# Optimization experiments

Measured on AMD Instinct MI355X. Metric: run time of the kernel, lower is better.

The kernel has to match this reference:

```python
import jax, jax.numpy as jnp
import numpy as np

B, DEC, ENC, HID, UNITS = 4, 256, 1024, 512, 128


def setup_inputs() -> dict:
    key = jax.random.key(0)
    k1, k2, k3, k4, k5, k6 = jax.random.split(key, 6)
    query = jax.random.normal(k1, (B, DEC, HID), dtype=jnp.float32)
    value = jax.random.normal(k2, (B, ENC, HID), dtype=jnp.float32)
    mask = jax.random.bernoulli(k3, 0.9, (B, ENC))  # bool, True = keep
    # Dense(units, use_bias=False) kernels, glorot-ish scaling
    W1 = jax.random.normal(k4, (HID, UNITS), dtype=jnp.float32) * (1.0 / np.sqrt(HID))
    W2 = jax.random.normal(k5, (HID, UNITS), dtype=jnp.float32) * (1.0 / np.sqrt(HID))
    # AdditiveAttention use_scale=True: learned per-unit scale vector
    scale = jax.random.normal(k6, (UNITS,), dtype=jnp.float32) * (1.0 / np.sqrt(UNITS))
    return {"query": query, "value": value, "mask": mask, "W1": W1, "W2": W2, "scale": scale}


def reference(query, value, mask, W1, W2, scale):
    # query: (B, DEC, HID), value: (B, ENC, HID), mask: (B, ENC) bool
    q = jnp.einsum("bqh,hu->bqu", query, W1)   # (B, DEC, U)
    k = jnp.einsum("beh,hu->beu", value, W2)   # (B, ENC, U)
    # Bahdanau additive score: sum_u scale_u * tanh(q + k)  -> (B, DEC, ENC)
    scores = jnp.einsum("bqeu,u->bqe", jnp.tanh(q[:, :, None, :] + k[:, None, :, :]), scale)
    neg = jnp.asarray(-1e9, scores.dtype)
    scores = jnp.where(mask[:, None, :], scores, neg)
    attention_weights = jax.nn.softmax(scores, axis=-1)   # (B, DEC, ENC)
    context_vector = jnp.einsum("bqe,beh->bqh", attention_weights, value)  # (B, DEC, HID)
    # query_mask is all-ones in the original module -> no-op on output
    return (context_vector, attention_weights)
```

## Files before the change

### kernel.cpp

```cpp
#include <hip/hip_runtime.h>
#include <cstddef>

#define B     4
#define DEC   256
#define ENC   1024
#define HID   512
#define UNITS 128

#define PROJ_SCALE 2.8853900817779268f

__global__ __launch_bounds__(256) void proj_kernel(
    const float* __restrict__ query, const float* __restrict__ value,
    const float* __restrict__ W1,    const float* __restrict__ W2,
    float* __restrict__ qbuf,        float* __restrict__ kbufT)
{
    __shared__ float part[4][8][UNITS];

    const int tid  = threadIdx.x;
    const int lane = tid & 63;
    const int wv   = __builtin_amdgcn_readfirstlane(tid >> 6);
    const int row0g = blockIdx.x * 8;
    const bool isQ = row0g < B * DEC;
    const float* X = isQ ? query : value;
    const float* W = isQ ? W1 : W2;
    const int row0 = isQ ? row0g : row0g - B * DEC;
    const int h0   = wv * 128;

    float acc0[8], acc1[8];
    #pragma unroll
    for (int r = 0; r < 8; ++r) { acc0[r] = 0.f; acc1[r] = 0.f; }

    const float* Xb = X + (size_t)row0 * HID + h0;
    const float* Wb = W + (size_t)h0 * UNITS;

    float wa[4], wb[4];
    #pragma unroll
    for (int j = 0; j < 4; ++j) {
        wa[j] = Wb[j * UNITS + lane];
        wb[j] = Wb[j * UNITS + 64 + lane];
    }

    for (int h = 0; h < 128; h += 4) {
        const int hp = (h + 4 < 128) ? h + 4 : h;
        float na[4], nb[4];
        #pragma unroll
        for (int j = 0; j < 4; ++j) {
            na[j] = Wb[(hp + j) * UNITS + lane];
            nb[j] = Wb[(hp + j) * UNITS + 64 + lane];
        }
        #pragma unroll
        for (int r = 0; r < 8; ++r) {
            const float4 xv = *(const float4*)(Xb + r * HID + h);
            acc0[r] += xv.x*wa[0] + xv.y*wa[1] + xv.z*wa[2] + xv.w*wa[3];
            acc1[r] += xv.x*wb[0] + xv.y*wb[1] + xv.z*wb[2] + xv.w*wb[3];
        }
        #pragma unroll
        for (int j = 0; j < 4; ++j) { wa[j] = na[j]; wb[j] = nb[j]; }
    }

    #pragma unroll
    for (int r = 0; r < 8; ++r) {
        part[wv][r][lane]      = acc0[r];
        part[wv][r][64 + lane] = acc1[r];
    }
    __syncthreads();

    #pragma unroll
    for (int k = 0; k < 4; ++k) {
        const int idx = tid + k * 256;
        const int r = idx >> 7, u = idx & (UNITS - 1);
        const float s = PROJ_SCALE *
            ((part[0][r][u] + part[1][r][u]) + (part[2][r][u] + part[3][r][u]));
        const int row = row0 + r;
        if (isQ) {
            qbuf[(size_t)row * UNITS + u] = s;
        } else {
            const int bb = row >> 10, e = row & (ENC - 1);
            const int c = u >> 2, j = u & 3;
            kbufT[((size_t)bb * 32 * ENC + (size_t)c * ENC + e) * 4 + j] = s;
        }
    }
}

__device__ __forceinline__ float sig_r(float a) {
    return __builtin_amdgcn_rcpf(1.f + __builtin_amdgcn_exp2f(a));
}

__global__ __launch_bounds__(1024) void score_kernel(
    const float* __restrict__ qbuf, const float* __restrict__ kbufT,
    const int* __restrict__ mask,   const float* __restrict__ scale,
    float* __restrict__ attn_out)
{
    const int bi  = blockIdx.x;
    const int b   = (bi >> 1) & 3;
    const int dq0 = (((bi >> 3) << 1) | (bi & 1)) * 2;
    const int tid = threadIdx.x;

    float S0 = 0.f;
    for (int j = 0; j < UNITS; j += 4) {
        const float4 sv = *(const float4*)(scale + j);
        S0 += (sv.x + sv.y) + (sv.z + sv.w);
    }

    const float* q0 = qbuf + (size_t)(b * DEC + dq0) * UNITS;
    const float* q1 = q0 + UNITS;
    const float* kc = kbufT + (size_t)b * 32 * ENC * 4 + (size_t)tid * 4;

    float t0 = 0.f, t1 = 0.f;

    float4 kv0 = *(const float4*)(kc + (size_t)0 * ENC * 4);
    float4 kv1 = *(const float4*)(kc + (size_t)1 * ENC * 4);
    float4 kv2 = *(const float4*)(kc + (size_t)2 * ENC * 4);
    float4 kv3 = *(const float4*)(kc + (size_t)3 * ENC * 4);

    for (int i = 0; i < 32; i += 4) {
        const int ip = (i + 4 < 32) ? (i + 4) : i;
        float4 n0 = *(const float4*)(kc + (size_t)(ip + 0) * ENC * 4);
        float4 n1 = *(const float4*)(kc + (size_t)(ip + 1) * ENC * 4);
        float4 n2 = *(const float4*)(kc + (size_t)(ip + 2) * ENC * 4);
        float4 n3 = *(const float4*)(kc + (size_t)(ip + 3) * ENC * 4);

        #pragma unroll
        for (int j = 0; j < 4; ++j) {
            const float4 kv = (j == 0) ? kv0 : (j == 1) ? kv1 : (j == 2) ? kv2 : kv3;
            const int ii = i + j;
            const float4 qa = *(const float4*)(q0 + ii * 4);
            const float4 qb = *(const float4*)(q1 + ii * 4);
            const float4 sv = *(const float4*)(scale + ii * 4);
            t0 += sv.x * sig_r(qa.x + kv.x);
            t0 += sv.y * sig_r(qa.y + kv.y);
            t0 += sv.z * sig_r(qa.z + kv.z);
            t0 += sv.w * sig_r(qa.w + kv.w);
            t1 += sv.x * sig_r(qb.x + kv.x);
            t1 += sv.y * sig_r(qb.y + kv.y);
            t1 += sv.z * sig_r(qb.z + kv.z);
            t1 += sv.w * sig_r(qb.w + kv.w);
        }
        kv0 = n0; kv1 = n1; kv2 = n2; kv3 = n3;
    }

    const int m = mask[b * ENC + tid];
    const float s0 = m ? (S0 - 2.f * t0) : -1e9f;
    const float s1 = m ? (S0 - 2.f * t1) : -1e9f;

    __shared__ float redm[2][16];
    __shared__ float reds[2][16];
    const int lane = tid & 63, wv = tid >> 6;

    float lm0 = s0, lm1 = s1;
    #pragma unroll
    for (int off = 32; off > 0; off >>= 1) {
        lm0 = fmaxf(lm0, __shfl_down(lm0, off, 64));
        lm1 = fmaxf(lm1, __shfl_down(lm1, off, 64));
    }
    if (lane == 0) { redm[0][wv] = lm0; redm[1][wv] = lm1; }
    __syncthreads();
    float gm0 = redm[0][0], gm1 = redm[1][0];
    #pragma unroll
    for (int w = 1; w < 16; ++w) {
        gm0 = fmaxf(gm0, redm[0][w]);
        gm1 = fmaxf(gm1, redm[1][w]);
    }

    const float w0 = __expf(s0 - gm0);
    const float w1 = __expf(s1 - gm1);
    float ls0 = w0, ls1 = w1;
    #pragma unroll
    for (int off = 32; off > 0; off >>= 1) {
        ls0 += __shfl_down(ls0, off, 64);
        ls1 += __shfl_down(ls1, off, 64);
    }
    if (lane == 0) { reds[0][wv] = ls0; reds[1][wv] = ls1; }
    __syncthreads();
    float gs0 = 0.f, gs1 = 0.f;
    #pragma unroll
    for (int w = 0; w < 16; ++w) { gs0 += reds[0][w]; gs1 += reds[1][w]; }
    const float inv0 = __builtin_amdgcn_rcpf(gs0);
    const float inv1 = __builtin_amdgcn_rcpf(gs1);

    attn_out[(size_t)(b * DEC + dq0) * ENC + tid]     = w0 * inv0;
    attn_out[(size_t)(b * DEC + dq0 + 1) * ENC + tid] = w1 * inv1;
}

__global__ __launch_bounds__(512) void ctx_kernel(
    const float* __restrict__ attn, const float* __restrict__ value,
    float* __restrict__ ctx)
{
    __shared__ float attnS[8][ENC];
    __shared__ float part[8][8][128];

    const int bi   = blockIdx.x;
    const int b    = (bi >> 1) & 3;
    const int idx  = ((bi >> 3) << 1) | (bi & 1);
    const int row0 = (idx >> 2) * 8;
    const int h0   = (idx & 3) * 128;
    const int tid  = threadIdx.x;
    const int lane = tid & 63;
    const int wv   = __builtin_amdgcn_readfirstlane(tid >> 6);

    const float* ab = attn + (size_t)(b * DEC + row0) * ENC;
    #pragma unroll
    for (int r = 0; r < 8; ++r) {
        const float2 v = *(const float2*)(ab + (size_t)r * ENC + tid * 2);
        *(float2*)&attnS[r][tid * 2] = v;
    }
    __syncthreads();

    float acc[8][2];
    #pragma unroll
    for (int r = 0; r < 8; ++r) { acc[r][0] = 0.f; acc[r][1] = 0.f; }

    const float* vb = value + (size_t)b * ENC * HID + h0 + lane * 2;
    const int e0 = wv * 128;

    float2 va[4];
    #pragma unroll
    for (int j = 0; j < 4; ++j)
        va[j] = *(const float2*)(vb + (size_t)(e0 + j) * HID);

    for (int g = 0; g < 32; ++g) {
        const int gp = (g + 1 < 32) ? g + 1 : g;
        float2 vn[4];
        #pragma unroll
        for (int j = 0; j < 4; ++j)
            vn[j] = *(const float2*)(vb + (size_t)(e0 + gp * 4 + j) * HID);

        const int eg = e0 + g * 4;
        float4 w4[8];
        #pragma unroll
        for (int r = 0; r < 8; ++r)
            w4[r] = *(const float4*)&attnS[r][eg];

        #pragma unroll
        for (int j = 0; j < 4; ++j) {
            const float2 v2 = va[j];
            #pragma unroll
            for (int r = 0; r < 8; ++r) {
                const float w = ((const float*)&w4[r])[j];
                acc[r][0] += w * v2.x;
                acc[r][1] += w * v2.y;
            }
        }
        #pragma unroll
        for (int j = 0; j < 4; ++j) va[j] = vn[j];
    }

    #pragma unroll
    for (int r = 0; r < 8; ++r)
        *(float2*)&part[wv][r][lane * 2] = make_float2(acc[r][0], acc[r][1]);
    __syncthreads();

    #pragma unroll
    for (int k = 0; k < 2; ++k) {
        const int idx2 = tid + k * 512;
        const int r = idx2 >> 7, hh = idx2 & 127;
        float s = 0.f;
        #pragma unroll
        for (int w = 0; w < 8; ++w) s += part[w][r][hh];
        ctx[(size_t)(b * DEC + row0 + r) * HID + h0 + hh] = s;
    }
}

extern "C" void kernel_launch(void* const* d_in, const int* in_sizes, int n_in,
                              void* d_out, int out_size, void* d_ws, size_t ws_size,
                              hipStream_t stream) {
    const float* query = (const float*)d_in[0];
    const float* value = (const float*)d_in[1];
    const int*   mask  = (const int*)  d_in[2];
    const float* W1    = (const float*)d_in[3];
    const float* W2    = (const float*)d_in[4];
    const float* scale = (const float*)d_in[5];

    float* qbuf  = (float*)d_ws;
    float* kbufT = qbuf + (size_t)B * DEC * UNITS;

    float* ctx_out  = (float*)d_out;
    float* attn_out = ctx_out + (size_t)B * DEC * HID;

    proj_kernel <<<640,  256, 0, stream>>>(query, value, W1, W2, qbuf, kbufT);
    score_kernel<<<512, 1024, 0, stream>>>(qbuf, kbufT, mask, scale, attn_out);
    ctx_kernel  <<<512,  512, 0, stream>>>(attn_out, value, ctx_out);
}
```

Before: 148.3 us.

## Precompute exp of projections so scores need one rcp per term, four rows per block

The projection kernel now stores exp2 of the scaled q and k projections. The score kernel can then form 1+exp(q+k) as a single fma of the two stored exponentials, which drops the per-element exp2 and keeps only the reciprocal. The score kernel also processes four decoder rows per block instead of two, halving the grid so each k load is reused across more rows. The trade-off is a risk of overflow or precision loss when the exponentials are multiplied for large projection magnitudes, plus higher register pressure per thread.

```diff
diff --git a/kernel.cpp b/kernel.cpp
--- a/kernel.cpp
+++ b/kernel.cpp
@@ -71,19 +71,16 @@
         const int r = idx >> 7, u = idx & (UNITS - 1);
         const float s = PROJ_SCALE *
             ((part[0][r][u] + part[1][r][u]) + (part[2][r][u] + part[3][r][u]));
+        const float z = __builtin_amdgcn_exp2f(s);
         const int row = row0 + r;
         if (isQ) {
-            qbuf[(size_t)row * UNITS + u] = s;
+            qbuf[(size_t)row * UNITS + u] = z;
         } else {
             const int bb = row >> 10, e = row & (ENC - 1);
             const int c = u >> 2, j = u & 3;
-            kbufT[((size_t)bb * 32 * ENC + (size_t)c * ENC + e) * 4 + j] = s;
-        }
-    }
-}
-
-__device__ __forceinline__ float sig_r(float a) {
-    return __builtin_amdgcn_rcpf(1.f + __builtin_amdgcn_exp2f(a));
+            kbufT[((size_t)bb * 32 * ENC + (size_t)c * ENC + e) * 4 + j] = z;
+        }
+    }
 }
 
 __global__ __launch_bounds__(1024) void score_kernel(
@@ -93,7 +90,7 @@
 {
     const int bi  = blockIdx.x;
     const int b   = (bi >> 1) & 3;
-    const int dq0 = (((bi >> 3) << 1) | (bi & 1)) * 2;
+    const int dq0 = (((bi >> 3) << 1) | (bi & 1)) * 4;
     const int tid = threadIdx.x;
 
     float S0 = 0.f;
@@ -103,83 +100,94 @@
     }
 
     const float* q0 = qbuf + (size_t)(b * DEC + dq0) * UNITS;
-    const float* q1 = q0 + UNITS;
     const float* kc = kbufT + (size_t)b * 32 * ENC * 4 + (size_t)tid * 4;
 
-    float t0 = 0.f, t1 = 0.f;
-
-    float4 kv0 = *(const float4*)(kc + (size_t)0 * ENC * 4);
-    float4 kv1 = *(const float4*)(kc + (size_t)1 * ENC * 4);
-    float4 kv2 = *(const float4*)(kc + (size_t)2 * ENC * 4);
-    float4 kv3 = *(const float4*)(kc + (size_t)3 * ENC * 4);
-
-    for (int i = 0; i < 32; i += 4) {
-        const int ip = (i + 4 < 32) ? (i + 4) : i;
-        float4 n0 = *(const float4*)(kc + (size_t)(ip + 0) * ENC * 4);
-        float4 n1 = *(const float4*)(kc + (size_t)(ip + 1) * ENC * 4);
-        float4 n2 = *(const float4*)(kc + (size_t)(ip + 2) * ENC * 4);
-        float4 n3 = *(const float4*)(kc + (size_t)(ip + 3) * ENC * 4);
-
-        #pragma unroll
-        for (int j = 0; j < 4; ++j) {
-            const float4 kv = (j == 0) ? kv0 : (j == 1) ? kv1 : (j == 2) ? kv2 : kv3;
-            const int ii = i + j;
-            const float4 qa = *(const float4*)(q0 + ii * 4);
-            const float4 qb = *(const float4*)(q1 + ii * 4);
-            const float4 sv = *(const float4*)(scale + ii * 4);
-            t0 += sv.x * sig_r(qa.x + kv.x);
-            t0 += sv.y * sig_r(qa.y + kv.y);
-            t0 += sv.z * sig_r(qa.z + kv.z);
-            t0 += sv.w * sig_r(qa.w + kv.w);
-            t1 += sv.x * sig_r(qb.x + kv.x);
-            t1 += sv.y * sig_r(qb.y + kv.y);
-            t1 += sv.z * sig_r(qb.z + kv.z);
-            t1 += sv.w * sig_r(qb.w + kv.w);
-        }
-        kv0 = n0; kv1 = n1; kv2 = n2; kv3 = n3;
+    float t0 = 0.f, t1 = 0.f, t2 = 0.f, t3 = 0.f;
+
+    float4 kv = *(const float4*)kc;
+    for (int i = 0; i < 32; ++i) {
+        float4 nkv;
+        if (i + 1 < 32) nkv = *(const float4*)(kc + (size_t)(i + 1) * ENC * 4);
+        const float4 sv = *(const float4*)(scale + i * 4);
+        const float4 qa = *(const float4*)(q0 + 0 * UNITS + i * 4);
+        const float4 qb = *(const float4*)(q0 + 1 * UNITS + i * 4);
+        const float4 qc = *(const float4*)(q0 + 2 * UNITS + i * 4);
+        const float4 qd = *(const float4*)(q0 + 3 * UNITS + i * 4);
+
+        t0 += sv.x * __builtin_amdgcn_rcpf(fmaf(qa.x, kv.x, 1.f));
+        t0 += sv.y * __builtin_amdgcn_rcpf(fmaf(qa.y, kv.y, 1.f));
+        t0 += sv.z * __builtin_amdgcn_rcpf(fmaf(qa.z, kv.z, 1.f));
+        t0 += sv.w * __builtin_amdgcn_rcpf(fmaf(qa.w, kv.w, 1.f));
+        t1 += sv.x * __builtin_amdgcn_rcpf(fmaf(qb.x, kv.x, 1.f));
+        t1 += sv.y * __builtin_amdgcn_rcpf(fmaf(qb.y, kv.y, 1.f));
+        t1 += sv.z * __builtin_amdgcn_rcpf(fmaf(qb.z, kv.z, 1.f));
+        t1 += sv.w * __builtin_amdgcn_rcpf(fmaf(qb.w, kv.w, 1.f));
+        t2 += sv.x * __builtin_amdgcn_rcpf(fmaf(qc.x, kv.x, 1.f));
+        t2 += sv.y * __builtin_amdgcn_rcpf(fmaf(qc.y, kv.y, 1.f));
+        t2 += sv.z * __builtin_amdgcn_rcpf(fmaf(qc.z, kv.z, 1.f));
+        t2 += sv.w * __builtin_amdgcn_rcpf(fmaf(qc.w, kv.w, 1.f));
+        t3 += sv.x * __builtin_amdgcn_rcpf(fmaf(qd.x, kv.x, 1.f));
+        t3 += sv.y * __builtin_amdgcn_rcpf(fmaf(qd.y, kv.y, 1.f));
+        t3 += sv.z * __builtin_amdgcn_rcpf(fmaf(qd.z, kv.z, 1.f));
+        t3 += sv.w * __builtin_amdgcn_rcpf(fmaf(qd.w, kv.w, 1.f));
+
+        if (i + 1 < 32) kv = nkv;
     }
 
     const int m = mask[b * ENC + tid];
-    const float s0 = m ? (S0 - 2.f * t0) : -1e9f;
-    const float s1 = m ? (S0 - 2.f * t1) : -1e9f;
-
-    __shared__ float redm[2][16];
-    __shared__ float reds[2][16];
+    float s[4];
+    s[0] = m ? (S0 - 2.f * t0) : -1e9f;
+    s[1] = m ? (S0 - 2.f * t1) : -1e9f;
+    s[2] = m ? (S0 - 2.f * t2) : -1e9f;
+    s[3] = m ? (S0 - 2.f * t3) : -1e9f;
+
+    __shared__ float redm[4][16];
+    __shared__ float reds[4][16];
     const int lane = tid & 63, wv = tid >> 6;
 
-    float lm0 = s0, lm1 = s1;
+    float lm[4] = {s[0], s[1], s[2], s[3]};
     #pragma unroll
     for (int off = 32; off > 0; off >>= 1) {
-        lm0 = fmaxf(lm0, __shfl_down(lm0, off, 64));
-        lm1 = fmaxf(lm1, __shfl_down(lm1, off, 64));
-    }
-    if (lane == 0) { redm[0][wv] = lm0; redm[1][wv] = lm1; }
-    __syncthreads();
-    float gm0 = redm[0][0], gm1 = redm[1][0];
-    #pragma unroll
-    for (int w = 1; w < 16; ++w) {
-        gm0 = fmaxf(gm0, redm[0][w]);
-        gm1 = fmaxf(gm1, redm[1][w]);
-    }
-
-    const float w0 = __expf(s0 - gm0);
-    const float w1 = __expf(s1 - gm1);
-    float ls0 = w0, ls1 = w1;
+        #pragma unroll
+        for (int r = 0; r < 4; ++r)
+            lm[r] = fmaxf(lm[r], __shfl_down(lm[r], off, 64));
+    }
+    if (lane == 0) {
+        #pragma unroll
+        for (int r = 0; r < 4; ++r) redm[r][wv] = lm[r];
+    }
+    __syncthreads();
+    float gm[4];
+    #pragma unroll
+    for (int r = 0; r < 4; ++r) {
+        float g = redm[r][0];
+        #pragma unroll
+        for (int w = 1; w < 16; ++w) g = fmaxf(g, redm[r][w]);
+        gm[r] = g;
+    }
+
+    float wgt[4], ls[4];
+    #pragma unroll
+    for (int r = 0; r < 4; ++r) { wgt[r] = __expf(s[r] - gm[r]); ls[r] = wgt[r]; }
     #pragma unroll
     for (int off = 32; off > 0; off >>= 1) {
-        ls0 += __shfl_down(ls0, off, 64);
-        ls1 += __shfl_down(ls1, off, 64);
-    }
-    if (lane == 0) { reds[0][wv] = ls0; reds[1][wv] = ls1; }
-    __syncthreads();
-    float gs0 = 0.f, gs1 = 0.f;
-    #pragma unroll
-    for (int w = 0; w < 16; ++w) { gs0 += reds[0][w]; gs1 += reds[1][w]; }
-    const float inv0 = __builtin_amdgcn_rcpf(gs0);
-    const float inv1 = __builtin_amdgcn_rcpf(gs1);
-
-    attn_out[(size_t)(b * DEC + dq0) * ENC + tid]     = w0 * inv0;
-    attn_out[(size_t)(b * DEC + dq0 + 1) * ENC + tid] = w1 * inv1;
+        #pragma unroll
+        for (int r = 0; r < 4; ++r)
+            ls[r] += __shfl_down(ls[r], off, 64);
+    }
+    if (lane == 0) {
+        #pragma unroll
+        for (int r = 0; r < 4; ++r) reds[r][wv] = ls[r];
+    }
+    __syncthreads();
+    #pragma unroll
+    for (int r = 0; r < 4; ++r) {
+        float g = 0.f;
+        #pragma unroll
+        for (int w = 0; w < 16; ++w) g += reds[r][w];
+        attn_out[(size_t)(b * DEC + dq0 + r) * ENC + tid] =
+            wgt[r] * __builtin_amdgcn_rcpf(g);
+    }
 }
 
 __global__ __launch_bounds__(512) void ctx_kernel(
@@ -278,6 +286,6 @@
     float* attn_out = ctx_out + (size_t)B * DEC * HID;
 
     proj_kernel <<<640,  256, 0, stream>>>(query, value, W1, W2, qbuf, kbufT);
-    score_kernel<<<512, 1024, 0, stream>>>(qbuf, kbufT, mask, scale, attn_out);
+    score_kernel<<<256, 1024, 0, stream>>>(qbuf, kbufT, mask, scale, attn_out);
     ctx_kernel  <<<512,  512, 0, stream>>>(attn_out, value, ctx_out);
 }
```

After: 134.8 us. 9.1% less time.
